# Kernel tuning notes

Measured on AMD Instinct MI355X. Metric: run time of the kernel, lower is better.

The kernel has to match this reference:

```python
import jax, jax.numpy as jnp
import numpy as np

N = 4096
IN_DIM, HID, OUT_DIM = 512, 256, 128
GAMMA = 6.0            # MCP weight truncation: w(y) = max(1 - y/gamma, 0)
LAM_HAT = 0.9
LAM = 1.0 / LAM_HAT - 1.0
PROP_STEPS = 10


def setup_inputs() -> dict:
    key = jax.random.key(0)
    k_a, k_f, k_w1, k_b1, k_w2, k_b2 = jax.random.split(key, 6)
    p = 32.0 / N  # avg degree ~32
    U = jax.random.uniform(k_a, (N, N))
    A = (U < p).astype(jnp.float32)
    A = jnp.maximum(A, A.T)                       # symmetric
    A = A * (1.0 - jnp.eye(N, dtype=jnp.float32))  # zero diagonal (loops added in forward)
    F = jax.random.normal(k_f, (N, IN_DIM), dtype=jnp.float32)
    W1 = jax.random.normal(k_w1, (IN_DIM, HID), dtype=jnp.float32) * 0.05
    b1 = jax.random.normal(k_b1, (HID,), dtype=jnp.float32) * 0.01
    W2 = jax.random.normal(k_w2, (HID, OUT_DIM), dtype=jnp.float32) * 0.05
    b2 = jax.random.normal(k_b2, (OUT_DIM,), dtype=jnp.float32) * 0.01
    return {"A": A, "F": F, "W1": W1, "b1": b1, "W2": W2, "b2": b2}


def reference(A, F, W1, b1, W2, b2):
    n = A.shape[0]
    # MLP (eval mode: dropout off)
    F0 = jnp.maximum(F @ W1 + b1, 0.0) @ W2 + b2          # [N, out_dim]
    # add self loops
    A = A + jnp.eye(n, dtype=A.dtype)
    D = A.sum(-1)                                          # [N]
    D_sq = jnp.sqrt(D)[:, None]                            # [N,1]
    A_t = A / (D_sq * D_sq.T)                              # sym-normalized adjacency
    diag = jnp.arange(n)
    Fc = F0
    for _ in range(PROP_STEPS):
        X = Fc / D_sq                                      # [N, d]
        sq = jnp.sum(X * X, axis=-1)                       # [N]
        Z = sq[:, None] + sq[None, :] - 2.0 * (X @ X.T)    # pairwise squared dist [N,N]
        Z = jax.lax.stop_gradient(jnp.maximum(Z, 0.0))
        Wm = jnp.maximum(1.0 - jnp.sqrt(Z) / GAMMA, 0.0)   # MCP IRLS weight
        Wm = Wm.at[diag, diag].set(0.0)
        Wm = jnp.where(jnp.isnan(Wm), 1.0, Wm)
        # quasi-Newton IRLS step
        Q = ((Wm * A).sum(-1) / D + LAM)[:, None]          # [N,1]
        Fc = (Wm * A_t) @ Fc / Q + LAM * F0 / Q
    return Fc
```

## Files before the change

kernel.cpp:

```cpp
#include <hip/hip_runtime.h>

#define NN 4096
#define IN_DIM 512
#define HID 256
#define OUT_DIM 128
#define MAXDEG 192
#define INV_GAMMA (1.0f / 6.0f)
#define LAM 0.11111111111111116f
#define PROP_STEPS 10

__global__ void k_analyze(const float* __restrict__ A, unsigned short* __restrict__ cols,
                          int* __restrict__ deg, float* __restrict__ DsqInv,
                          float* __restrict__ Dinv) {
    int wid = threadIdx.x >> 6, lane = threadIdx.x & 63;
    int row = blockIdx.x * 4 + wid;
    const float4* Ar = (const float4*)(A + (size_t)row * NN);
    unsigned short* crow = cols + (size_t)row * MAXDEG;
    int cnt = 0;
    float fsum = 0.f;
    for (int it = 0; it < NN / 256; ++it) {
        float4 v = Ar[it * 64 + lane];
        fsum += (v.x + v.y) + (v.z + v.w);
        int colbase = (it * 64 + lane) * 4;
        float comp[4] = {v.x, v.y, v.z, v.w};
#pragma unroll
        for (int c = 0; c < 4; ++c) {
            bool nz = (comp[c] != 0.f);
            unsigned long long m = __ballot(nz);
            if (nz) {
                int off = cnt + __popcll(m & ((1ull << lane) - 1ull));
                if (off < MAXDEG) crow[off] = (unsigned short)(colbase + c);
            }
            cnt += __popcll(m);
        }
    }
#pragma unroll
    for (int m = 1; m < 64; m <<= 1) fsum += __shfl_xor(fsum, m);
    if (lane == 0) {
        float D = fsum + 1.0f;
        deg[row] = cnt < MAXDEG ? cnt : MAXDEG;
        DsqInv[row] = 1.0f / sqrtf(D);
        Dinv[row] = 1.0f / D;
    }
}

__global__ __launch_bounds__(256) void k_mlp(const float* __restrict__ F,
                      const float* __restrict__ W1, const float* __restrict__ b1,
                      const float* __restrict__ W2, const float* __restrict__ b2,
                      const float* __restrict__ DsqInv,
                      float* __restrict__ F0, float* __restrict__ X0) {
    __shared__ __align__(16) float sF[8 * IN_DIM];
    __shared__ __align__(16) float sW[32 * 256];
    __shared__ __align__(16) float sH[8 * HID];
    int r0 = blockIdx.x * 8;
    int t = threadIdx.x;
    float4* sF4 = (float4*)sF;
    float4* sW4 = (float4*)sW;
#pragma unroll
    for (int i = 0; i < 4; ++i) {
        int idx = i * 256 + t;
        int r = idx >> 7, q = idx & 127;
        sF4[r * 128 + q] = *(const float4*)&F[(size_t)(r0 + r) * IN_DIM + 4 * q];
    }
    {
        int cq = t & 63, rg = t >> 6;
        float4 accA = make_float4(0.f, 0.f, 0.f, 0.f);
        float4 accB = make_float4(0.f, 0.f, 0.f, 0.f);
        for (int kt = 0; kt < IN_DIM / 32; ++kt) {
            __syncthreads();
#pragma unroll
            for (int i = 0; i < 8; ++i) {
                int idx = i * 256 + t;
                int kr = idx >> 6, q = idx & 63;
                sW4[kr * 64 + q] = *(const float4*)&W1[(size_t)(kt * 32 + kr) * HID + 4 * q];
            }
            __syncthreads();
#pragma unroll
            for (int g4 = 0; g4 < 8; ++g4) {
                float4 w0 = sW4[(4 * g4 + 0) * 64 + cq];
                float4 w1 = sW4[(4 * g4 + 1) * 64 + cq];
                float4 w2 = sW4[(4 * g4 + 2) * 64 + cq];
                float4 w3 = sW4[(4 * g4 + 3) * 64 + cq];
                float4 fA = sF4[(2 * rg) * 128 + kt * 8 + g4];
                float4 fB = sF4[(2 * rg + 1) * 128 + kt * 8 + g4];
                accA.x = fmaf(fA.x, w0.x, accA.x); accA.y = fmaf(fA.x, w0.y, accA.y);
                accA.z = fmaf(fA.x, w0.z, accA.z); accA.w = fmaf(fA.x, w0.w, accA.w);
                accA.x = fmaf(fA.y, w1.x, accA.x); accA.y = fmaf(fA.y, w1.y, accA.y);
                accA.z = fmaf(fA.y, w1.z, accA.z); accA.w = fmaf(fA.y, w1.w, accA.w);
                accA.x = fmaf(fA.z, w2.x, accA.x); accA.y = fmaf(fA.z, w2.y, accA.y);
                accA.z = fmaf(fA.z, w2.z, accA.z); accA.w = fmaf(fA.z, w2.w, accA.w);
                accA.x = fmaf(fA.w, w3.x, accA.x); accA.y = fmaf(fA.w, w3.y, accA.y);
                accA.z = fmaf(fA.w, w3.z, accA.z); accA.w = fmaf(fA.w, w3.w, accA.w);
                accB.x = fmaf(fB.x, w0.x, accB.x); accB.y = fmaf(fB.x, w0.y, accB.y);
                accB.z = fmaf(fB.x, w0.z, accB.z); accB.w = fmaf(fB.x, w0.w, accB.w);
                accB.x = fmaf(fB.y, w1.x, accB.x); accB.y = fmaf(fB.y, w1.y, accB.y);
                accB.z = fmaf(fB.y, w1.z, accB.z); accB.w = fmaf(fB.y, w1.w, accB.w);
                accB.x = fmaf(fB.z, w2.x, accB.x); accB.y = fmaf(fB.z, w2.y, accB.y);
                accB.z = fmaf(fB.z, w2.z, accB.z); accB.w = fmaf(fB.z, w2.w, accB.w);
                accB.x = fmaf(fB.w, w3.x, accB.x); accB.y = fmaf(fB.w, w3.y, accB.y);
                accB.z = fmaf(fB.w, w3.z, accB.z); accB.w = fmaf(fB.w, w3.w, accB.w);
            }
        }
        float4 b = *(const float4*)&b1[4 * cq];
        float4 ha, hb;
        ha.x = fmaxf(accA.x + b.x, 0.f); ha.y = fmaxf(accA.y + b.y, 0.f);
        ha.z = fmaxf(accA.z + b.z, 0.f); ha.w = fmaxf(accA.w + b.w, 0.f);
        hb.x = fmaxf(accB.x + b.x, 0.f); hb.y = fmaxf(accB.y + b.y, 0.f);
        hb.z = fmaxf(accB.z + b.z, 0.f); hb.w = fmaxf(accB.w + b.w, 0.f);
        *(float4*)&sH[(2 * rg) * HID + 4 * cq] = ha;
        *(float4*)&sH[(2 * rg + 1) * HID + 4 * cq] = hb;
    }
    {
        int c = t & 127, half = t >> 7;
        float acc2[4] = {0.f, 0.f, 0.f, 0.f};
        for (int kt = 0; kt < HID / 32; ++kt) {
            __syncthreads();
#pragma unroll
            for (int i = 0; i < 4; ++i) {
                int idx = i * 256 + t;
                int kr = idx >> 5, q = idx & 31;
                sW4[kr * 32 + q] = *(const float4*)&W2[(size_t)(kt * 32 + kr) * OUT_DIM + 4 * q];
            }
            __syncthreads();
#pragma unroll
            for (int kk = 0; kk < 32; ++kk) {
                int k = kt * 32 + kk;
                float w = sW[kk * 128 + c];
#pragma unroll
                for (int r = 0; r < 4; ++r)
                    acc2[r] = fmaf(sH[(half * 4 + r) * HID + k], w, acc2[r]);
            }
        }
        float b = b2[c];
#pragma unroll
        for (int r = 0; r < 4; ++r) {
            int row = r0 + half * 4 + r;
            float v = acc2[r] + b;
            F0[(size_t)row * OUT_DIM + c] = v;
            X0[(size_t)row * OUT_DIM + c] = v * DsqInv[row];
        }
    }
}

__global__ void k_sq0(const float* __restrict__ X, float* __restrict__ sq) {
    int wid = threadIdx.x >> 6, lane = threadIdx.x & 63;
    int row = blockIdx.x * 4 + wid;
    float2 x = ((const float2*)X)[row * 64 + lane];
    float s = x.x * x.x + x.y * x.y;
#pragma unroll
    for (int m = 1; m < 64; m <<= 1) s += __shfl_xor(s, m);
    if (lane == 0) sq[row] = s;
}

__global__ __launch_bounds__(256, 6) void k_prop(const float* __restrict__ X,
                       const float* __restrict__ F0,
                       const unsigned short* __restrict__ cols, const int* __restrict__ deg,
                       const float* __restrict__ DsqInv, const float* __restrict__ Dinv,
                       const float* __restrict__ sq_in,
                       float* __restrict__ Xout, float* __restrict__ sq_out,
                       float* __restrict__ FcOut, int final_step) {
    __shared__ unsigned short sCols[2][MAXDEG];
    __shared__ float sPart[2][16][130];
    __shared__ float sQw[2][2];
    int t = threadIdx.x;
    int wave = t >> 6, lane = t & 63;
    int rl = wave >> 1, half = wave & 1;
    int row = blockIdx.x * 2 + rl;
    int g = lane >> 3, oc = lane & 7;
    int dg = deg[row];
    {
        int idx = half * 64 + lane;
        for (int e = idx; e < dg; e += 128)
            sCols[rl][e] = cols[(size_t)row * MAXDEG + e];
    }
    float sqi = sq_in[row];
    const float4* Xi4 = (const float4*)(X + (size_t)row * 128 + oc * 16);
    float4 xi0 = Xi4[0], xi1 = Xi4[1], xi2 = Xi4[2], xi3 = Xi4[3];
    __syncthreads();
    float4 a0 = make_float4(0.f,0.f,0.f,0.f), a1 = make_float4(0.f,0.f,0.f,0.f);
    float4 a2 = make_float4(0.f,0.f,0.f,0.f), a3 = make_float4(0.f,0.f,0.f,0.f);
    float qacc = 0.f;
    int nch = (dg + 15) >> 4;
    for (int ch = 0; ch < nch; ++ch) {
        int e = ch * 16 + half * 8 + g;
        bool act = e < dg;
        int j = (int)sCols[rl][act ? e : 0];
        const float4* Xj4 = (const float4*)(X + (size_t)j * 128 + oc * 16);
        float4 c0 = Xj4[0], c1 = Xj4[1], c2 = Xj4[2], c3 = Xj4[3];
        float sqj = sq_in[j];
        float pA = 0.f, pB = 0.f;
        pA = fmaf(xi0.x, c0.x, pA); pB = fmaf(xi0.y, c0.y, pB);
        pA = fmaf(xi0.z, c0.z, pA); pB = fmaf(xi0.w, c0.w, pB);
        pA = fmaf(xi1.x, c1.x, pA); pB = fmaf(xi1.y, c1.y, pB);
        pA = fmaf(xi1.z, c1.z, pA); pB = fmaf(xi1.w, c1.w, pB);
        pA = fmaf(xi2.x, c2.x, pA); pB = fmaf(xi2.y, c2.y, pB);
        pA = fmaf(xi2.z, c2.z, pA); pB = fmaf(xi2.w, c2.w, pB);
        pA = fmaf(xi3.x, c3.x, pA); pB = fmaf(xi3.y, c3.y, pB);
        pA = fmaf(xi3.z, c3.z, pA); pB = fmaf(xi3.w, c3.w, pB);
        float p = pA + pB;
        p += __shfl_xor(p, 1);
        p += __shfl_xor(p, 2);
        p += __shfl_xor(p, 4);
        float z = fmaxf(sqi + sqj - 2.f * p, 0.f);
        float w = fmaxf(1.f - sqrtf(z) * INV_GAMMA, 0.f);
        w = act ? w : 0.f;
        qacc += w;
        a0.x = fmaf(w, c0.x, a0.x); a0.y = fmaf(w, c0.y, a0.y);
        a0.z = fmaf(w, c0.z, a0.z); a0.w = fmaf(w, c0.w, a0.w);
        a1.x = fmaf(w, c1.x, a1.x); a1.y = fmaf(w, c1.y, a1.y);
        a1.z = fmaf(w, c1.z, a1.z); a1.w = fmaf(w, c1.w, a1.w);
        a2.x = fmaf(w, c2.x, a2.x); a2.y = fmaf(w, c2.y, a2.y);
        a2.z = fmaf(w, c2.z, a2.z); a2.w = fmaf(w, c2.w, a2.w);
        a3.x = fmaf(w, c3.x, a3.x); a3.y = fmaf(w, c3.y, a3.y);
        a3.z = fmaf(w, c3.z, a3.z); a3.w = fmaf(w, c3.w, a3.w);
    }
    int slot = half * 8 + g;
    *(float4*)&sPart[rl][slot][oc * 16 + 0]  = a0;
    *(float4*)&sPart[rl][slot][oc * 16 + 4]  = a1;
    *(float4*)&sPart[rl][slot][oc * 16 + 8]  = a2;
    *(float4*)&sPart[rl][slot][oc * 16 + 12] = a3;
    if (oc == 0) sPart[rl][slot][128] = qacc;
    __syncthreads();
    int rl2 = t >> 7, d = t & 127;
    int row2 = blockIdx.x * 2 + rl2;
    float acc = 0.f, qs = 0.f;
#pragma unroll
    for (int s = 0; s < 16; ++s) {
        acc += sPart[rl2][s][d];
        qs  += sPart[rl2][s][128];
    }
    float dsi = DsqInv[row2];
    float invQ = 1.f / (qs * Dinv[row2] + LAM);
    float o = (dsi * acc + LAM * F0[(size_t)row2 * 128 + d]) * invQ;
    if (final_step) {
        FcOut[(size_t)row2 * 128 + d] = o;
    } else {
        float x = o * dsi;
        Xout[(size_t)row2 * 128 + d] = x;
        float ss = x * x;
#pragma unroll
        for (int m = 1; m < 64; m <<= 1) ss += __shfl_xor(ss, m);
        if (lane == 0) sQw[rl2][wave & 1] = ss;
    }
    __syncthreads();
    if (!final_step && t < 2) sq_out[blockIdx.x * 2 + t] = sQw[t][0] + sQw[t][1];
}

extern "C" void kernel_launch(void* const* d_in, const int* in_sizes, int n_in,
                              void* d_out, int out_size, void* d_ws, size_t ws_size,
                              hipStream_t stream) {
    const float *A = nullptr, *F = nullptr, *W1 = nullptr, *b1 = nullptr,
                *W2 = nullptr, *b2 = nullptr;
    for (int i = 0; i < n_in; i++) {
        switch (in_sizes[i]) {
            case NN * NN:        A  = (const float*)d_in[i]; break;
            case NN * IN_DIM:    F  = (const float*)d_in[i]; break;
            case IN_DIM * HID:   W1 = (const float*)d_in[i]; break;
            case HID:            b1 = (const float*)d_in[i]; break;
            case HID * OUT_DIM:  W2 = (const float*)d_in[i]; break;
            case OUT_DIM:        b2 = (const float*)d_in[i]; break;
            default: break;
        }
    }
    float* out = (float*)d_out;

    char* ws = (char*)d_ws;
    float* F0     = (float*)ws; ws += (size_t)NN * OUT_DIM * 4;
    float* XA     = (float*)ws; ws += (size_t)NN * OUT_DIM * 4;
    float* XB     = (float*)ws; ws += (size_t)NN * OUT_DIM * 4;
    float* DsqInv = (float*)ws; ws += (size_t)NN * 4;
    float* Dinv   = (float*)ws; ws += (size_t)NN * 4;
    float* sqA    = (float*)ws; ws += (size_t)NN * 4;
    float* sqB    = (float*)ws; ws += (size_t)NN * 4;
    int*   deg    = (int*)ws;   ws += (size_t)NN * 4;
    unsigned short* cols = (unsigned short*)ws; ws += (size_t)NN * MAXDEG * 2;

    hipLaunchKernelGGL(k_analyze, dim3(NN / 4), dim3(256), 0, stream, A, cols, deg, DsqInv, Dinv);
    hipLaunchKernelGGL(k_mlp, dim3(NN / 8), dim3(256), 0, stream,
                       F, W1, b1, W2, b2, DsqInv, F0, XA);
    hipLaunchKernelGGL(k_sq0, dim3(NN / 4), dim3(256), 0, stream, XA, sqA);

    float* Xc = XA; float* Xn = XB;
    float* sqc = sqA; float* sqn = sqB;
    for (int step = 0; step < PROP_STEPS; step++) {
        int fin = (step == PROP_STEPS - 1) ? 1 : 0;
        hipLaunchKernelGGL(k_prop, dim3(NN / 2), dim3(256), 0, stream,
                           Xc, F0, cols, deg, DsqInv, Dinv, sqc, Xn, sqn, out, fin);
        float* t1 = Xc; Xc = Xn; Xn = t1;
        float* t2 = sqc; sqc = sqn; sqn = t2;
    }
}
```

Before: 318.8 us.

## Assign one wave per row in propagation kernel and interleave neighbor loads

Each k_prop block now handles four rows with one wavefront per row, where previously two waves split each row's edges. Neighbor-row loads are interleaved so the eight lanes of a group read consecutive float4s, which improves coalescing. Per-row sums are finished inside the wave, removing the second barrier and the cross-wave sq merge. The edge loop now has twice as many iterations per wave, and the launch-bounds occupancy hint was removed, which may change register allocation.

```diff
diff --git a/kernel.cpp b/kernel.cpp
--- a/kernel.cpp
+++ b/kernel.cpp
@@ -152,41 +152,35 @@
     if (lane == 0) sq[row] = s;
 }
 
-__global__ __launch_bounds__(256, 6) void k_prop(const float* __restrict__ X,
+__global__ __launch_bounds__(256) void k_prop(const float* __restrict__ X,
                        const float* __restrict__ F0,
                        const unsigned short* __restrict__ cols, const int* __restrict__ deg,
                        const float* __restrict__ DsqInv, const float* __restrict__ Dinv,
                        const float* __restrict__ sq_in,
                        float* __restrict__ Xout, float* __restrict__ sq_out,
                        float* __restrict__ FcOut, int final_step) {
-    __shared__ unsigned short sCols[2][MAXDEG];
-    __shared__ float sPart[2][16][130];
-    __shared__ float sQw[2][2];
+    __shared__ unsigned short sCols[4][MAXDEG];
+    __shared__ __align__(16) float sPart[4][8][136];
     int t = threadIdx.x;
-    int wave = t >> 6, lane = t & 63;
-    int rl = wave >> 1, half = wave & 1;
-    int row = blockIdx.x * 2 + rl;
+    int wid = t >> 6, lane = t & 63;
+    int row = blockIdx.x * 4 + wid;
     int g = lane >> 3, oc = lane & 7;
     int dg = deg[row];
-    {
-        int idx = half * 64 + lane;
-        for (int e = idx; e < dg; e += 128)
-            sCols[rl][e] = cols[(size_t)row * MAXDEG + e];
-    }
+    for (int e = lane; e < dg; e += 64) sCols[wid][e] = cols[(size_t)row * MAXDEG + e];
     float sqi = sq_in[row];
-    const float4* Xi4 = (const float4*)(X + (size_t)row * 128 + oc * 16);
-    float4 xi0 = Xi4[0], xi1 = Xi4[1], xi2 = Xi4[2], xi3 = Xi4[3];
+    const float4* Xr4 = (const float4*)(X + (size_t)row * 128);
+    float4 xi0 = Xr4[oc], xi1 = Xr4[8 + oc], xi2 = Xr4[16 + oc], xi3 = Xr4[24 + oc];
     __syncthreads();
     float4 a0 = make_float4(0.f,0.f,0.f,0.f), a1 = make_float4(0.f,0.f,0.f,0.f);
     float4 a2 = make_float4(0.f,0.f,0.f,0.f), a3 = make_float4(0.f,0.f,0.f,0.f);
     float qacc = 0.f;
-    int nch = (dg + 15) >> 4;
+    int nch = (dg + 7) >> 3;
     for (int ch = 0; ch < nch; ++ch) {
-        int e = ch * 16 + half * 8 + g;
+        int e = ch * 8 + g;
         bool act = e < dg;
-        int j = (int)sCols[rl][act ? e : 0];
-        const float4* Xj4 = (const float4*)(X + (size_t)j * 128 + oc * 16);
-        float4 c0 = Xj4[0], c1 = Xj4[1], c2 = Xj4[2], c3 = Xj4[3];
+        int j = (int)sCols[wid][act ? e : 0];
+        const float4* Xj4 = (const float4*)(X + (size_t)j * 128);
+        float4 c0 = Xj4[oc], c1 = Xj4[8 + oc], c2 = Xj4[16 + oc], c3 = Xj4[24 + oc];
         float sqj = sq_in[j];
         float pA = 0.f, pB = 0.f;
         pA = fmaf(xi0.x, c0.x, pA); pB = fmaf(xi0.y, c0.y, pB);
@@ -214,36 +208,38 @@
         a3.x = fmaf(w, c3.x, a3.x); a3.y = fmaf(w, c3.y, a3.y);
         a3.z = fmaf(w, c3.z, a3.z); a3.w = fmaf(w, c3.w, a3.w);
     }
-    int slot = half * 8 + g;
-    *(float4*)&sPart[rl][slot][oc * 16 + 0]  = a0;
-    *(float4*)&sPart[rl][slot][oc * 16 + 4]  = a1;
-    *(float4*)&sPart[rl][slot][oc * 16 + 8]  = a2;
-    *(float4*)&sPart[rl][slot][oc * 16 + 12] = a3;
-    if (oc == 0) sPart[rl][slot][128] = qacc;
+    {
+        float* part = &sPart[wid][g][0];
+        *(float4*)&part[ 0 + 4 * oc] = a0;
+        *(float4*)&part[32 + 4 * oc] = a1;
+        *(float4*)&part[64 + 4 * oc] = a2;
+        *(float4*)&part[96 + 4 * oc] = a3;
+        if (oc == 0) part[128] = qacc;
+    }
     __syncthreads();
-    int rl2 = t >> 7, d = t & 127;
-    int row2 = blockIdx.x * 2 + rl2;
-    float acc = 0.f, qs = 0.f;
-#pragma unroll
-    for (int s = 0; s < 16; ++s) {
-        acc += sPart[rl2][s][d];
-        qs  += sPart[rl2][s][128];
-    }
-    float dsi = DsqInv[row2];
-    float invQ = 1.f / (qs * Dinv[row2] + LAM);
-    float o = (dsi * acc + LAM * F0[(size_t)row2 * 128 + d]) * invQ;
+    int d0 = lane * 2;
+    float accX = 0.f, accY = 0.f, qs = 0.f;
+#pragma unroll
+    for (int s = 0; s < 8; ++s) {
+        float2 v = *(const float2*)&sPart[wid][s][d0];
+        accX += v.x; accY += v.y;
+        qs += sPart[wid][s][128];
+    }
+    float dsi = DsqInv[row];
+    float invQ = 1.f / (qs * Dinv[row] + LAM);
+    float2 f0 = *(const float2*)&F0[(size_t)row * 128 + d0];
+    float ox = (dsi * accX + LAM * f0.x) * invQ;
+    float oy = (dsi * accY + LAM * f0.y) * invQ;
     if (final_step) {
-        FcOut[(size_t)row2 * 128 + d] = o;
+        *(float2*)&FcOut[(size_t)row * 128 + d0] = make_float2(ox, oy);
     } else {
-        float x = o * dsi;
-        Xout[(size_t)row2 * 128 + d] = x;
-        float ss = x * x;
+        float xx = ox * dsi, xy = oy * dsi;
+        *(float2*)&Xout[(size_t)row * 128 + d0] = make_float2(xx, xy);
+        float ss = xx * xx + xy * xy;
 #pragma unroll
         for (int m = 1; m < 64; m <<= 1) ss += __shfl_xor(ss, m);
-        if (lane == 0) sQw[rl2][wave & 1] = ss;
-    }
-    __syncthreads();
-    if (!final_step && t < 2) sq_out[blockIdx.x * 2 + t] = sQw[t][0] + sQw[t][1];
+        if (lane == 0) sq_out[row] = ss;
+    }
 }
 
 extern "C" void kernel_launch(void* const* d_in, const int* in_sizes, int n_in,
@@ -284,7 +280,7 @@
     float* sqc = sqA; float* sqn = sqB;
     for (int step = 0; step < PROP_STEPS; step++) {
         int fin = (step == PROP_STEPS - 1) ? 1 : 0;
-        hipLaunchKernelGGL(k_prop, dim3(NN / 2), dim3(256), 0, stream,
+        hipLaunchKernelGGL(k_prop, dim3(NN / 4), dim3(256), 0, stream,
                            Xc, F0, cols, deg, DsqInv, Dinv, sqc, Xn, sqn, out, fin);
         float* t1 = Xc; Xc = Xn; Xn = t1;
         float* t2 = sqc; sqc = sqn; sqn = t2;
```

Result: faster. 264.0 us (-17.2%).
